# Kernel optimization log

Hardware: AMD Instinct MI355X
Metric: run time of the kernel (lower is better)

The kernel has to match this reference:

```python
import jax, jax.numpy as jnp
import numpy as np

WINDOW_SIZE = 8
NUM_HEADS = 6
SHIFT_SIZE = 0


def rel_pos_log(ws):
    # torch.meshgrid default is 'ij' indexing
    coords = jnp.stack(jnp.meshgrid(jnp.arange(ws), jnp.arange(ws), indexing='ij'))  # [2,ws,ws]
    flat = coords.reshape(2, -1)                      # [2, N]
    rel = flat[:, :, None] - flat[:, None, :]          # [2, N, N]
    rel = rel.transpose(1, 2, 0).astype(jnp.float32)   # [N, N, 2]
    return jnp.sign(rel) * jnp.log1p(jnp.abs(rel))


def setup_inputs() -> dict:
    key = jax.random.key(0)
    k0, k1, k2, k3 = jax.random.split(key, 4)
    B_, N, dim, H = 2048, WINDOW_SIZE * WINDOW_SIZE, 192, NUM_HEADS
    qkv = jax.random.normal(k0, (B_, N, 3 * dim), dtype=jnp.float32)
    qkv_mfif = jax.random.normal(k1, (B_, N, 3 * dim), dtype=jnp.float32)
    W1 = jax.random.normal(k2, (2, 256), dtype=jnp.float32) * 0.1
    b1 = jnp.zeros((256,), dtype=jnp.float32)
    W2 = jax.random.normal(k3, (256, H), dtype=jnp.float32) * 0.1
    b2 = jnp.zeros((H,), dtype=jnp.float32)
    return {"qkv": qkv, "qkv_mfif": qkv_mfif, "W1": W1, "b1": b1,
            "W2": W2, "b2": b2, "trainingTag": 2}


def _split_heads(t, H):
    B_, N, C3 = t.shape
    dim = C3 // 3
    hd = dim // H
    t = t.reshape(B_, N, 3, H, hd).transpose(2, 0, 3, 1, 4)  # [3, B_, H, N, hd]
    return t[0], t[1], t[2]


def _forward(qkv, qkv_mfif, W1, b1, W2, b2, trainingTag):
    sg = jax.lax.stop_gradient
    H = NUM_HEADS
    B_, N, C3 = qkv.shape
    dim = C3 // 3
    hd = dim // H
    scale = hd ** (-0.5)

    q, k, v = _split_heads(qkv, H)
    qm, km, vm = _split_heads(qkv_mfif, H)

    # relative position bias from tiny MLP: [N,N,2] -> [N,N,H] -> [H,N,N]
    rp = rel_pos_log(WINDOW_SIZE)
    bias = jax.nn.relu(rp @ W1 + b1) @ W2 + b2
    bias = bias.transpose(2, 0, 1)[None]  # [1,H,N,N]

    if trainingTag == 2:
        q = sg(q * scale)
        qm = qm * scale
        if SHIFT_SIZE == 0:
            attn = sg(jnp.einsum('bhnd,bhmd->bhnm', qm, k))
        else:
            attn = sg(jnp.einsum('bhnd,bhmd->bhnm', q, k))
        attn_m = jnp.einsum('bhnd,bhmd->bhnm', qm, km)
        attn = sg(jax.nn.softmax(attn + sg(bias), axis=-1))
        attn_m = jax.nn.softmax(attn_m + bias, axis=-1)
        x_ivif = sg(jnp.einsum('bhnm,bhmd->bhnd', attn, v).transpose(0, 2, 1, 3).reshape(B_, N, dim))
        x_mfif = jnp.einsum('bhnm,bhmd->bhnd', attn_m, vm).transpose(0, 2, 1, 3).reshape(B_, N, dim)
    else:  # trainingTag == 1
        q = q * scale
        qm = sg(qm * scale)
        attn = jnp.einsum('bhnd,bhmd->bhnm', q, k)
        if SHIFT_SIZE == 0:
            attn_m = sg(jnp.einsum('bhnd,bhmd->bhnm', q, km))
        else:
            attn_m = sg(jnp.einsum('bhnd,bhmd->bhnm', qm, km))
        attn = jax.nn.softmax(attn + bias, axis=-1)
        attn_m = sg(jax.nn.softmax(attn_m + bias, axis=-1))
        x_ivif = jnp.einsum('bhnm,bhmd->bhnd', attn, v).transpose(0, 2, 1, 3).reshape(B_, N, dim)
        x_mfif = sg(jnp.einsum('bhnm,bhmd->bhnd', attn_m, vm).transpose(0, 2, 1, 3).reshape(B_, N, dim))
    return x_ivif, x_mfif


def reference(qkv, qkv_mfif, W1, b1, W2, b2, trainingTag):
    return _forward(qkv, qkv_mfif, W1, b1, W2, b2, trainingTag)
```

## Files before the change

kernel.cpp:

```cpp
#include <hip/hip_runtime.h>


typedef float  f32x4  __attribute__((ext_vector_type(4)));
typedef short  bf16x8 __attribute__((ext_vector_type(8)));
typedef unsigned short u16x8 __attribute__((ext_vector_type(8)));
typedef unsigned short u16x4 __attribute__((ext_vector_type(4)));

__device__ __forceinline__ unsigned short f2bf(float f) {
  unsigned int u = __builtin_bit_cast(unsigned int, f);
  unsigned int r = (u + 0x7FFFu + ((u >> 16) & 1u)) >> 16;
  return (unsigned short)r;
}

__global__ void bias_mlp_kernel(const float* __restrict__ W1,
                                const float* __restrict__ b1,
                                const float* __restrict__ W2,
                                const float* __restrict__ b2,
                                float* __restrict__ bias_ws) {
  int idx  = blockIdx.x * 256 + threadIdx.x;
  int reg  = idx & 3;
  int lane = (idx >> 2) & 63;
  int tile = (idx >> 8) & 15;
  int h    = idx >> 12;
  int mt = tile >> 2, nt = tile & 3;
  int n = nt * 16 + (lane & 15);
  int m = mt * 16 + (lane >> 4) * 4 + reg;
  float dr = (float)((n >> 3) - (m >> 3));
  float dc = (float)((n & 7) - (m & 7));
  float fr = copysignf(log1pf(fabsf(dr)), dr);
  float fc = copysignf(log1pf(fabsf(dc)), dc);
  float acc = b2[h];
  for (int jj = 0; jj < 256; ++jj) {
    float hid = fmaf(fr, W1[jj], fmaf(fc, W1[256 + jj], b1[jj]));
    hid = fmaxf(hid, 0.0f);
    acc = fmaf(hid, W2[jj * 6 + h], acc);
  }
  bias_ws[idx] = acc;
}

__global__ __launch_bounds__(256, 4)
void wattn_kernel(const float* __restrict__ qkv,
                  const float* __restrict__ mfif,
                  const float* __restrict__ bias_ws,
                  const int*   __restrict__ tagp,
                  float* __restrict__ out) {
  const int bid  = blockIdx.x;
  const int h    = bid % 6;
  const int b    = bid / 6;
  const int tid  = threadIdx.x;
  const int lane = tid & 63;
  const int w    = tid >> 6;
  const int j    = lane & 15;
  const int g    = lane >> 4;

  __shared__ unsigned short qm_s[64][40];
  __shared__ unsigned short k_s [64][40];
  __shared__ unsigned short km_s[64][40];
  __shared__ unsigned short vT_s[2][32][72];
  __shared__ unsigned short P_s [64][72];

  const int tag = *tagp;
  const float* qsrc = (tag == 2) ? mfif : qkv;
  const size_t base = (size_t)b * 36864;
  const float scale = 0.17677669529663687f;

  {
    const int n = tid >> 2, seg = tid & 3;
    const float* pq = qsrc + base + (size_t)n * 576 +       h * 32 + seg * 8;
    const float* pk = qkv  + base + (size_t)n * 576 + 192 + h * 32 + seg * 8;
    const float* pm = mfif + base + (size_t)n * 576 + 192 + h * 32 + seg * 8;
    f32x4 q0 = *(const f32x4*)pq;  f32x4 q1 = *(const f32x4*)(pq + 4);
    f32x4 k0 = *(const f32x4*)pk;  f32x4 k1 = *(const f32x4*)(pk + 4);
    f32x4 m0 = *(const f32x4*)pm;  f32x4 m1 = *(const f32x4*)(pm + 4);
    u16x8 oq, ok, om;
#pragma unroll
    for (int e = 0; e < 4; ++e) {
      oq[e] = f2bf(q0[e] * scale); oq[e + 4] = f2bf(q1[e] * scale);
      ok[e] = f2bf(k0[e]);         ok[e + 4] = f2bf(k1[e]);
      om[e] = f2bf(m0[e]);         om[e + 4] = f2bf(m1[e]);
    }
    *(u16x8*)&qm_s[n][seg * 8] = oq;
    *(u16x8*)&k_s [n][seg * 8] = ok;
    *(u16x8*)&km_s[n][seg * 8] = om;
  }
  {
    const int d  = tid & 31;
    const int m0 = (tid >> 5) * 8;
    const int ms = m0 ^ (((d >> 3) & 3) << 3);
    const float* pv  = qkv  + base + 384 + h * 32 + d;
    const float* pvm = mfif + base + 384 + h * 32 + d;
    u16x8 ov, om;
#pragma unroll
    for (int e = 0; e < 8; ++e) {
      ov[e] = f2bf(pv [(size_t)(m0 + e) * 576]);
      om[e] = f2bf(pvm[(size_t)(m0 + e) * 576]);
    }
    *(u16x8*)&vT_s[0][d][ms] = ov;
    *(u16x8*)&vT_s[1][d][ms] = om;
  }
  __syncthreads();

  bf16x8 bq = *(const bf16x8*)&qm_s[16 * w + j][g * 8];
  f32x4 bias4[4];
#pragma unroll
  for (int mt = 0; mt < 4; ++mt)
    bias4[mt] = *(const f32x4*)&bias_ws[(((h * 16) + mt * 4 + w) * 64 + lane) * 4];

#pragma unroll
  for (int s = 0; s < 2; ++s) {
    const unsigned short (*Ks)[40] = (s == 0) ? k_s : km_s;

    f32x4 acc[4];
#pragma unroll
    for (int mt = 0; mt < 4; ++mt) {
      bf16x8 ak = *(const bf16x8*)&Ks[mt * 16 + j][g * 8];
      acc[mt] = __builtin_amdgcn_mfma_f32_16x16x32_bf16(ak, bq, bias4[mt], 0, 0, 0);
    }

    float mx = -3.0e38f;
#pragma unroll
    for (int mt = 0; mt < 4; ++mt)
#pragma unroll
      for (int r = 0; r < 4; ++r) mx = fmaxf(mx, acc[mt][r]);
    mx = fmaxf(mx, __shfl_xor(mx, 16));
    mx = fmaxf(mx, __shfl_xor(mx, 32));
    float p[16];
    float sum = 0.0f;
#pragma unroll
    for (int mt = 0; mt < 4; ++mt)
#pragma unroll
      for (int r = 0; r < 4; ++r) {
        float e = __expf(acc[mt][r] - mx);
        p[mt * 4 + r] = e;
        sum += e;
      }
    sum += __shfl_xor(sum, 16);
    sum += __shfl_xor(sum, 32);
    const float inv = 1.0f / sum;

#pragma unroll
    for (int mt = 0; mt < 4; ++mt) {
      u16x4 pw;
#pragma unroll
      for (int r = 0; r < 4; ++r) pw[r] = f2bf(p[mt * 4 + r] * inv);
      *(u16x4*)&P_s[16 * w + j][mt * 16 + g * 4] = pw;
    }

    f32x4 xo[2] = {{0.f, 0.f, 0.f, 0.f}, {0.f, 0.f, 0.f, 0.f}};
#pragma unroll
    for (int kt = 0; kt < 2; ++kt) {
      bf16x8 ap = *(const bf16x8*)&P_s[16 * w + j][kt * 32 + g * 8];
#pragma unroll
      for (int dt = 0; dt < 2; ++dt) {
        const int d   = 16 * dt + j;
        const int mrd = (32 * kt + 8 * g) ^ (((d >> 3) & 3) << 3);
        bf16x8 bv = *(const bf16x8*)&vT_s[s][d][mrd];
        xo[dt] = __builtin_amdgcn_mfma_f32_16x16x32_bf16(ap, bv, xo[dt], 0, 0, 0);
      }
    }

    float* ob = out + (size_t)s * 25165824 + (size_t)b * 12288 + h * 32;
#pragma unroll
    for (int dt = 0; dt < 2; ++dt)
#pragma unroll
      for (int r = 0; r < 4; ++r)
        ob[(16 * w + g * 4 + r) * 192 + dt * 16 + j] = xo[dt][r];
  }
}

extern "C" void kernel_launch(void* const* d_in, const int* in_sizes, int n_in,
                              void* d_out, int out_size, void* d_ws, size_t ws_size,
                              hipStream_t stream) {
  const float* qkv  = (const float*)d_in[0];
  const float* mfif = (const float*)d_in[1];
  const float* W1   = (const float*)d_in[2];
  const float* b1   = (const float*)d_in[3];
  const float* W2   = (const float*)d_in[4];
  const float* b2   = (const float*)d_in[5];
  const int*   tag  = (const int*)d_in[6];
  float* out     = (float*)d_out;
  float* bias_ws = (float*)d_ws;

  hipLaunchKernelGGL(bias_mlp_kernel, dim3(96), dim3(256), 0, stream,
                     W1, b1, W2, b2, bias_ws);
  hipLaunchKernelGGL(wattn_kernel, dim3(12288), dim3(256), 0, stream,
                     qkv, mfif, bias_ws, tag, out);
}
```

Before: 152.8 us.

## Load Q straight into registers, drop swizzle, repad LDS, raise occupancy bound

Each wave now loads its query fragment from global memory directly into MFMA registers, so the Q shared-memory staging buffer is gone. The XOR swizzle on V-transpose is replaced by plain padding (row strides 36 and 66). The barrier moves after the bias loads, and the launch bound rises from 4 to 6 blocks per SM. The goal is less LDS traffic and footprint plus more overlap, but the new strides leave the 16-byte vector LDS accesses only partly aligned, which may split or serialize them.

Measured after the change: 157.4 us. +3.0%, slower.

```diff
diff --git a/kernel.cpp b/kernel.cpp
--- a/kernel.cpp
+++ b/kernel.cpp
@@ -38,7 +38,7 @@
   bias_ws[idx] = acc;
 }
 
-__global__ __launch_bounds__(256, 4)
+__global__ __launch_bounds__(256, 6)
 void wattn_kernel(const float* __restrict__ qkv,
                   const float* __restrict__ mfif,
                   const float* __restrict__ bias_ws,
@@ -53,40 +53,48 @@
   const int j    = lane & 15;
   const int g    = lane >> 4;
 
-  __shared__ unsigned short qm_s[64][40];
-  __shared__ unsigned short k_s [64][40];
-  __shared__ unsigned short km_s[64][40];
-  __shared__ unsigned short vT_s[2][32][72];
-  __shared__ unsigned short P_s [64][72];
+  __shared__ unsigned short k_s [64][36];
+  __shared__ unsigned short km_s[64][36];
+  __shared__ unsigned short vT_s[2][32][66];
+  __shared__ unsigned short P_s [64][66];
 
   const int tag = *tagp;
   const float* qsrc = (tag == 2) ? mfif : qkv;
   const size_t base = (size_t)b * 36864;
   const float scale = 0.17677669529663687f;
 
+  bf16x8 bq;
+  {
+    const float* pq = qsrc + base + (size_t)(16 * w + j) * 576 + h * 32 + g * 8;
+    f32x4 q0 = *(const f32x4*)pq;
+    f32x4 q1 = *(const f32x4*)(pq + 4);
+    u16x8 oq;
+#pragma unroll
+    for (int e = 0; e < 4; ++e) {
+      oq[e]     = f2bf(q0[e] * scale);
+      oq[e + 4] = f2bf(q1[e] * scale);
+    }
+    bq = __builtin_bit_cast(bf16x8, oq);
+  }
+
   {
     const int n = tid >> 2, seg = tid & 3;
-    const float* pq = qsrc + base + (size_t)n * 576 +       h * 32 + seg * 8;
     const float* pk = qkv  + base + (size_t)n * 576 + 192 + h * 32 + seg * 8;
     const float* pm = mfif + base + (size_t)n * 576 + 192 + h * 32 + seg * 8;
-    f32x4 q0 = *(const f32x4*)pq;  f32x4 q1 = *(const f32x4*)(pq + 4);
     f32x4 k0 = *(const f32x4*)pk;  f32x4 k1 = *(const f32x4*)(pk + 4);
     f32x4 m0 = *(const f32x4*)pm;  f32x4 m1 = *(const f32x4*)(pm + 4);
-    u16x8 oq, ok, om;
+    u16x8 ok, om;
 #pragma unroll
     for (int e = 0; e < 4; ++e) {
-      oq[e] = f2bf(q0[e] * scale); oq[e + 4] = f2bf(q1[e] * scale);
-      ok[e] = f2bf(k0[e]);         ok[e + 4] = f2bf(k1[e]);
-      om[e] = f2bf(m0[e]);         om[e + 4] = f2bf(m1[e]);
+      ok[e] = f2bf(k0[e]);  ok[e + 4] = f2bf(k1[e]);
+      om[e] = f2bf(m0[e]);  om[e + 4] = f2bf(m1[e]);
     }
-    *(u16x8*)&qm_s[n][seg * 8] = oq;
     *(u16x8*)&k_s [n][seg * 8] = ok;
     *(u16x8*)&km_s[n][seg * 8] = om;
   }
   {
     const int d  = tid & 31;
     const int m0 = (tid >> 5) * 8;
-    const int ms = m0 ^ (((d >> 3) & 3) << 3);
     const float* pv  = qkv  + base + 384 + h * 32 + d;
     const float* pvm = mfif + base + 384 + h * 32 + d;
     u16x8 ov, om;
@@ -95,20 +103,20 @@
       ov[e] = f2bf(pv [(size_t)(m0 + e) * 576]);
       om[e] = f2bf(pvm[(size_t)(m0 + e) * 576]);
     }
-    *(u16x8*)&vT_s[0][d][ms] = ov;
-    *(u16x8*)&vT_s[1][d][ms] = om;
+    *(u16x8*)&vT_s[0][d][m0] = ov;
+    *(u16x8*)&vT_s[1][d][m0] = om;
   }
-  __syncthreads();
 
-  bf16x8 bq = *(const bf16x8*)&qm_s[16 * w + j][g * 8];
   f32x4 bias4[4];
 #pragma unroll
   for (int mt = 0; mt < 4; ++mt)
     bias4[mt] = *(const f32x4*)&bias_ws[(((h * 16) + mt * 4 + w) * 64 + lane) * 4];
 
+  __syncthreads();
+
 #pragma unroll
   for (int s = 0; s < 2; ++s) {
-    const unsigned short (*Ks)[40] = (s == 0) ? k_s : km_s;
+    const unsigned short (*Ks)[36] = (s == 0) ? k_s : km_s;
 
     f32x4 acc[4];
 #pragma unroll
@@ -152,9 +160,7 @@
       bf16x8 ap = *(const bf16x8*)&P_s[16 * w + j][kt * 32 + g * 8];
 #pragma unroll
       for (int dt = 0; dt < 2; ++dt) {
-        const int d   = 16 * dt + j;
-        const int mrd = (32 * kt + 8 * g) ^ (((d >> 3) & 3) << 3);
-        bf16x8 bv = *(const bf16x8*)&vT_s[s][d][mrd];
+        bf16x8 bv = *(const bf16x8*)&vT_s[s][16 * dt + j][kt * 32 + g * 8];
         xo[dt] = __builtin_amdgcn_mfma_f32_16x16x32_bf16(ap, bv, xo[dt], 0, 0, 0);
       }
     }
```
